# Kernel optimization log

Measured on AMD Instinct MI355X. Metric: run time of the kernel, lower is better.

Reference implementation:

```python
import jax, jax.numpy as jnp
import numpy as np

L, D, H, F = 6, 768, 12, 3072   # layers, d_model, heads, mlp hidden
B, S = 2, 2048                   # batch, seq_len
DH = D // H                      # head dim
EPS = 1e-5


def _layer_norm(x, w, b):
    mu = jnp.mean(x, axis=-1, keepdims=True)
    var = jnp.mean(jnp.square(x - mu), axis=-1, keepdims=True)
    return (x - mu) * jax.lax.rsqrt(var + EPS) * w + b


def setup_inputs() -> dict:
    key = jax.random.key(0)
    ks = jax.random.split(key, 8)
    w = lambda k, shape: jax.random.normal(k, shape, dtype=jnp.float32) * 0.02
    return {
        "x": jax.random.normal(ks[0], (B, S, D), dtype=jnp.float32),
        # attention projections, stacked over layers; weights stored (d_in, d_out)
        "Wq": w(ks[1], (L, D, D)), "bq": jnp.zeros((L, D), jnp.float32),
        "Wk": w(ks[2], (L, D, D)), "bk": jnp.zeros((L, D), jnp.float32),
        "Wv": w(ks[3], (L, D, D)), "bv": jnp.zeros((L, D), jnp.float32),
        "Wo": w(ks[4], (L, D, D)), "bo": jnp.zeros((L, D), jnp.float32),
        "ln1_w": jnp.ones((L, D), jnp.float32), "ln1_b": jnp.zeros((L, D), jnp.float32),
        "W1": w(ks[5], (L, D, F)), "b1": jnp.zeros((L, F), jnp.float32),
        "W2": w(ks[6], (L, F, D)), "b2": jnp.zeros((L, D), jnp.float32),
        "ln2_w": jnp.ones((L, D), jnp.float32), "ln2_b": jnp.zeros((L, D), jnp.float32),
        "lnf_w": jnp.ones((D,), jnp.float32), "lnf_b": jnp.zeros((D,), jnp.float32),
    }


def reference(x, Wq, bq, Wk, bk, Wv, bv, Wo, bo, ln1_w, ln1_b,
              W1, b1, W2, b2, ln2_w, ln2_b, lnf_w, lnf_b):
    scale = DH ** (-0.5)
    for i in range(L):
        # pre-norm MSA block; NB: residual uses the normalized x, as in source
        xn = _layer_norm(x, ln1_w[i], ln1_b[i])
        q = (xn @ Wq[i] + bq[i]).reshape(B, S, H, DH).transpose(0, 2, 1, 3)
        k = (xn @ Wk[i] + bk[i]).reshape(B, S, H, DH).transpose(0, 2, 1, 3)
        v = (xn @ Wv[i] + bv[i]).reshape(B, S, H, DH).transpose(0, 2, 1, 3)
        att = jax.nn.softmax(scale * jnp.einsum('bhqd,bhkd->bhqk', q, k), axis=-1)
        out = jnp.einsum('bhqk,bhkd->bhqd', att, v)
        out = out.transpose(0, 2, 1, 3).reshape(B, S, D)
        x = xn + (out @ Wo[i] + bo[i])
        # pre-norm FFN block; residual uses the normalized x, as in source
        xn2 = _layer_norm(x, ln2_w[i], ln2_b[i])
        h = jax.nn.gelu(xn2 @ W1[i] + b1[i], approximate=False)
        x = xn2 + (h @ W2[i] + b2[i])
    return _layer_norm(x, lnf_w, lnf_b)
```

## Files before the change

### kernel.cpp

```cpp
#include <hip/hip_runtime.h>
#include <stdint.h>

typedef unsigned short u16;
typedef unsigned int   u32;

#define L_N  6
#define D_N  768
#define F_N  3072
#define H_N  12
#define B_N  2
#define S_N  2048
#define BS_N 4096
#define QKV_N 2304
#define CSC  0.18033688011112042f
#define DTHR 11.54f

using bf16x8 = __attribute__((ext_vector_type(8))) short;
using f32x4  = __attribute__((ext_vector_type(4))) float;
using f32x16 = __attribute__((ext_vector_type(16))) float;
using u32x2  = __attribute__((ext_vector_type(2))) unsigned int;

__device__ __forceinline__ u16 f2bf(float f) {
  u32 x = __builtin_bit_cast(u32, f);
  x += 0x7FFFu + ((x >> 16) & 1u);
  return (u16)(x >> 16);
}

__device__ __forceinline__ float bf2f(u16 v) {
  return __builtin_bit_cast(float, (u32)v << 16);
}

__device__ __forceinline__ u32 cvt_pk_bf16(float lo, float hi) {
  u32 r;
  asm("v_cvt_pk_bf16_f32 %0, %1, %2" : "=v"(r) : "v"(lo), "v"(hi));
  return r;
}

#define GLOAD16(g, l)                                                                     \
  __builtin_amdgcn_global_load_lds((const __attribute__((address_space(1))) void*)(g),    \
                                   (__attribute__((address_space(3))) void*)(l), 16, 0, 0)

__global__ __launch_bounds__(256) void transpose_cast_kernel(
    const float* __restrict__ in, u16* __restrict__ out, int K, int N,
    size_t out_lstride, int out_rowoff)
{
  __shared__ float tile[32][33];
  const int l  = blockIdx.z;
  const int n0 = blockIdx.x * 32, k0 = blockIdx.y * 32;
  const int tx = threadIdx.x & 31, ty = threadIdx.x >> 5;
  const float* src = in + (size_t)l * K * N;
  u16* dst = out + (size_t)l * out_lstride + (size_t)out_rowoff * K;
#pragma unroll
  for (int i = 0; i < 4; ++i)
    tile[ty + i * 8][tx] = src[(size_t)(k0 + ty + i * 8) * N + n0 + tx];
  __syncthreads();
#pragma unroll
  for (int i = 0; i < 4; ++i)
    dst[(size_t)(n0 + ty + i * 8) * K + k0 + tx] = f2bf(tile[tx][ty + i * 8]);
}

__global__ __launch_bounds__(256) void concat_bias_kernel(
    const float* __restrict__ bq, const float* __restrict__ bk,
    const float* __restrict__ bv, float* __restrict__ out)
{
  const int i = blockIdx.x * 256 + threadIdx.x;
  const int l = i / QKV_N, c = i - l * QKV_N;
  float v = (c < 768) ? bq[l * 768 + c]
          : (c < 1536) ? bk[l * 768 + c - 768]
                       : bv[l * 768 + c - 1536];
  out[i] = v;
}

template<bool BF16IN>
__global__ __launch_bounds__(256) void ln_kernel(
    const void* __restrict__ xv, const float* __restrict__ w, const float* __restrict__ b,
    float* __restrict__ outF, u16* __restrict__ outB)
{
  const int row = blockIdx.x, tid = threadIdx.x;
  float v[3];
  float s = 0.f;
  if (BF16IN) {
    const u16* xr = (const u16*)xv + (size_t)row * D_N;
#pragma unroll
    for (int i = 0; i < 3; ++i) { v[i] = bf2f(xr[tid + i * 256]); s += v[i]; }
  } else {
    const float* xr = (const float*)xv + (size_t)row * D_N;
#pragma unroll
    for (int i = 0; i < 3; ++i) { v[i] = xr[tid + i * 256]; s += v[i]; }
  }
  __shared__ float red[8];
  const int wave = tid >> 6, lane = tid & 63;
#pragma unroll
  for (int o = 32; o > 0; o >>= 1) s += __shfl_down(s, o, 64);
  if (lane == 0) red[wave] = s;
  __syncthreads();
  const float mu = (red[0] + red[1] + red[2] + red[3]) * (1.f / D_N);
  float d2 = 0.f;
#pragma unroll
  for (int i = 0; i < 3; ++i) { float d = v[i] - mu; d2 += d * d; }
#pragma unroll
  for (int o = 32; o > 0; o >>= 1) d2 += __shfl_down(d2, o, 64);
  if (lane == 0) red[4 + wave] = d2;
  __syncthreads();
  const float var = (red[4] + red[5] + red[6] + red[7]) * (1.f / D_N);
  const float rs = rsqrtf(var + 1e-5f);
#pragma unroll
  for (int i = 0; i < 3; ++i) {
    const int c = tid + i * 256;
    const float o = (v[i] - mu) * rs * w[c] + b[c];
    if (outF) outF[(size_t)row * D_N + c] = o;
    if (outB) outB[(size_t)row * D_N + c] = f2bf(o);
  }
}

template<bool GELU, bool OUTB, bool SCALEQ>
__global__ __launch_bounds__(256) void gemm_kernel(
    const u16* __restrict__ A, const u16* __restrict__ Wt,
    const float* __restrict__ bias,
    u16* __restrict__ outB, int M, int N, int K)
{
  __shared__ __align__(16) u16 As[2][128 * 32];
  __shared__ __align__(16) u16 Bs[2][128 * 32];
  const int tid  = threadIdx.x;
  const int wave = tid >> 6, lane = tid & 63;
  const int lr = lane & 15, lg = lane >> 4;
  const int row0 = blockIdx.x * 128, col0 = blockIdx.y * 128;
  const int wr = (wave >> 1) * 64, wc = (wave & 1) * 64;

  const int cb0 = wave * 64;
  const int cb1 = 256 + wave * 64;
  const int r0s = (cb0 + lane) >> 2, c0s = ((cb0 + lane) & 3) << 3;
  const int r1s = (cb1 + lane) >> 2, c1s = ((cb1 + lane) & 3) << 3;

  f32x4 acc[4][4] = {};

#define STAGE(cbuf, kk)                                                           \
  do {                                                                            \
    GLOAD16(A  + (size_t)(row0 + r0s) * K + (kk) + c0s, &As[cbuf][cb0 * 8]);      \
    GLOAD16(Wt + (size_t)(col0 + r0s) * K + (kk) + c0s, &Bs[cbuf][cb0 * 8]);      \
    GLOAD16(A  + (size_t)(row0 + r1s) * K + (kk) + c1s, &As[cbuf][cb1 * 8]);      \
    GLOAD16(Wt + (size_t)(col0 + r1s) * K + (kk) + c1s, &Bs[cbuf][cb1 * 8]);      \
  } while (0)

  STAGE(0, 0);
  __syncthreads();

  int c = 0;
  for (int k0 = 0; k0 < K; k0 += 32, c ^= 1) {
    if (k0 + 32 < K) STAGE(c ^ 1, k0 + 32);
    bf16x8 af[4], bfr[4];
#pragma unroll
    for (int m = 0; m < 4; ++m)
      af[m] = *(const bf16x8*)&As[c][(wr + m * 16 + lr) * 32 + lg * 8];
#pragma unroll
    for (int n = 0; n < 4; ++n)
      bfr[n] = *(const bf16x8*)&Bs[c][(wc + n * 16 + lr) * 32 + lg * 8];
    __builtin_amdgcn_s_setprio(1);
#pragma unroll
    for (int m = 0; m < 4; ++m)
#pragma unroll
      for (int n = 0; n < 4; ++n)
        acc[m][n] = __builtin_amdgcn_mfma_f32_16x16x32_bf16(af[m], bfr[n], acc[m][n], 0, 0, 0);
    __builtin_amdgcn_s_setprio(0);
    __syncthreads();
  }
#undef STAGE

#pragma unroll
  for (int m = 0; m < 4; ++m)
#pragma unroll
    for (int n = 0; n < 4; ++n) {
      const int col = col0 + wc + n * 16 + lr;
      const float bv = bias[col];
#pragma unroll
      for (int r = 0; r < 4; ++r) {
        const int row = row0 + wr + m * 16 + lg * 4 + r;
        float v = acc[m][n][r] + bv;
        if (GELU) v = 0.5f * v * (1.f + erff(v * 0.70710678118f));
        if (SCALEQ && col < 768) v *= CSC;
        const size_t idx = (size_t)row * N + col;
        if (OUTB) outB[idx] = f2bf(v);
      }
    }
}

__global__ __launch_bounds__(256) void gemm64_kernel(
    const u16* __restrict__ A, const u16* __restrict__ Wt,
    const float* __restrict__ bias, const u16* __restrict__ resid,
    u16* __restrict__ outB, int M, int N, int K)
{
  __shared__ __align__(16) u16 As[2][64 * 32];
  __shared__ __align__(16) u16 Bs[2][64 * 32];
  const int tid  = threadIdx.x;
  const int wave = tid >> 6, lane = tid & 63;
  const int lr = lane & 15, lg = lane >> 4;
  const int row0 = blockIdx.x * 64, col0 = blockIdx.y * 64;
  const int wr = (wave >> 1) * 32, wc = (wave & 1) * 32;

  const int cb = wave * 64;
  const int ch = cb + lane;
  const int rs = ch >> 2, cs = (ch & 3) << 3;

  f32x4 acc[2][2] = {};

#define STAGE64(cbuf, kk)                                                         \
  do {                                                                            \
    GLOAD16(A  + (size_t)(row0 + rs) * K + (kk) + cs, &As[cbuf][cb * 8]);         \
    GLOAD16(Wt + (size_t)(col0 + rs) * K + (kk) + cs, &Bs[cbuf][cb * 8]);         \
  } while (0)

  STAGE64(0, 0);
  __syncthreads();

  int c = 0;
  for (int k0 = 0; k0 < K; k0 += 32, c ^= 1) {
    if (k0 + 32 < K) STAGE64(c ^ 1, k0 + 32);
    bf16x8 af[2], bfr[2];
#pragma unroll
    for (int m = 0; m < 2; ++m)
      af[m] = *(const bf16x8*)&As[c][(wr + m * 16 + lr) * 32 + lg * 8];
#pragma unroll
    for (int n = 0; n < 2; ++n)
      bfr[n] = *(const bf16x8*)&Bs[c][(wc + n * 16 + lr) * 32 + lg * 8];
    __builtin_amdgcn_s_setprio(1);
#pragma unroll
    for (int m = 0; m < 2; ++m)
#pragma unroll
      for (int n = 0; n < 2; ++n)
        acc[m][n] = __builtin_amdgcn_mfma_f32_16x16x32_bf16(af[m], bfr[n], acc[m][n], 0, 0, 0);
    __builtin_amdgcn_s_setprio(0);
    __syncthreads();
  }
#undef STAGE64

#pragma unroll
  for (int m = 0; m < 2; ++m)
#pragma unroll
    for (int n = 0; n < 2; ++n) {
      const int col = col0 + wc + n * 16 + lr;
      const float bv = bias[col];
#pragma unroll
      for (int r = 0; r < 4; ++r) {
        const int row = row0 + wr + m * 16 + lg * 4 + r;
        const size_t idx = (size_t)row * N + col;
        outB[idx] = f2bf(acc[m][n][r] + bv + bf2f(resid[idx]));
      }
    }
}

__global__ __launch_bounds__(256) void attn_kernel(
    const u16* __restrict__ QKV, float* __restrict__ Opart, float* __restrict__ Ml)
{
  constexpr int LDQ = QKV_N;
  constexpr int NT  = S_N / 64;
  __shared__ __align__(16) u16 Ks [64 * 72];
  __shared__ __align__(16) u16 VTs[64 * 72];
  const int tid  = threadIdx.x;
  const int wave = tid >> 6, lane = tid & 63;
  const int l31 = lane & 31, l5 = lane >> 5;
  const int bh = blockIdx.y;
  const int b = bh / H_N, h = bh - b * H_N;
  const int q0 = blockIdx.x * 128;
  const int z  = blockIdx.z;
  const int t0 = z * (NT / 2), t1 = (z + 1) * (NT / 2);
  const size_t rowbase = (size_t)b * S_N * LDQ;
  const u16* Qg = QKV + rowbase + h * 64;
  const u16* Kg = QKV + rowbase + 768 + h * 64;
  const u16* Vg = QKV + rowbase + 1536 + h * 64;

  const int qrow = q0 + wave * 32 + l31;
  bf16x8 qf[4];
#pragma unroll
  for (int ks = 0; ks < 4; ++ks)
    qf[ks] = *(const bf16x8*)(Qg + (size_t)qrow * LDQ + ks * 16 + l5 * 8);

  f32x16 o0 = {}, o1 = {};
  float m = -1e30f, l = 0.f;

  const int kr = tid >> 2, kc = (tid & 3) * 16;
  const int pp = tid >> 3, cg = tid & 7;

  const u16* gk0 = Kg + (size_t)(t0 * 64 + kr) * LDQ + kc;
  const u16* gv0 = Vg + (size_t)(t0 * 64 + 2 * pp) * LDQ + cg * 8;
  uint4 nk0 = *(const uint4*)gk0, nk1 = *(const uint4*)(gk0 + 8);
  uint4 nv0 = *(const uint4*)gv0, nv1 = *(const uint4*)(gv0 + LDQ);

  for (int t = t0; t < t1; ++t) {
    __syncthreads();
    {
      *(uint4*)&Ks[kr * 72 + kc]     = nk0;
      *(uint4*)&Ks[kr * 72 + kc + 8] = nk1;
      const u16* a0 = (const u16*)&nv0;
      const u16* a1 = (const u16*)&nv1;
#pragma unroll
      for (int j = 0; j < 8; ++j) {
        const int jj = (j + cg) & 7;
        *(u32*)&VTs[(cg * 8 + jj) * 72 + 2 * pp] = (u32)a0[jj] | ((u32)a1[jj] << 16);
      }
    }
    __syncthreads();

    if (t + 1 < t1) {
      const u16* gk1 = Kg + (size_t)((t + 1) * 64 + kr) * LDQ + kc;
      const u16* gv1 = Vg + (size_t)((t + 1) * 64 + 2 * pp) * LDQ + cg * 8;
      nk0 = *(const uint4*)gk1; nk1 = *(const uint4*)(gk1 + 8);
      nv0 = *(const uint4*)gv1; nv1 = *(const uint4*)(gv1 + LDQ);
    }

    f32x16 sv0 = {}, sv1 = {};
    __builtin_amdgcn_s_setprio(1);
#pragma unroll
    for (int ks = 0; ks < 4; ++ks) {
      const bf16x8 kf0 = *(const bf16x8*)&Ks[(l31)      * 72 + ks * 16 + l5 * 8];
      const bf16x8 kf1 = *(const bf16x8*)&Ks[(32 + l31) * 72 + ks * 16 + l5 * 8];
      sv0 = __builtin_amdgcn_mfma_f32_32x32x16_bf16(kf0, qf[ks], sv0, 0, 0, 0);
      sv1 = __builtin_amdgcn_mfma_f32_32x32x16_bf16(kf1, qf[ks], sv1, 0, 0, 0);
    }
    __builtin_amdgcn_s_setprio(0);

    float mx = sv0[0];
#pragma unroll
    for (int i = 0; i < 16; ++i) mx = fmaxf(mx, sv0[i]);
#pragma unroll
    for (int i = 0; i < 16; ++i) mx = fmaxf(mx, sv1[i]);
    {
      const u32 mb = __builtin_bit_cast(u32, mx);
      const u32x2 rr = __builtin_amdgcn_permlane32_swap(mb, mb, false, false);
      mx = fmaxf(__builtin_bit_cast(float, rr[0]), __builtin_bit_cast(float, rr[1]));
    }
    if (!__all(mx - m <= DTHR)) {
      const float mn = fmaxf(m, mx);
      const float al = __builtin_amdgcn_exp2f(m - mn);
      m = mn;
      l *= al;
#pragma unroll
      for (int i = 0; i < 16; ++i) { o0[i] *= al; o1[i] *= al; }
    }
    float rs = 0.f;
#pragma unroll
    for (int i = 0; i < 16; ++i) {
      const float e = __builtin_amdgcn_exp2f(sv0[i] - m);
      sv0[i] = e; rs += e;
    }
#pragma unroll
    for (int i = 0; i < 16; ++i) {
      const float e = __builtin_amdgcn_exp2f(sv1[i] - m);
      sv1[i] = e; rs += e;
    }
    {
      const u32 sb = __builtin_bit_cast(u32, rs);
      const u32x2 rr = __builtin_amdgcn_permlane32_swap(sb, sb, false, false);
      rs = __builtin_bit_cast(float, rr[0]) + __builtin_bit_cast(float, rr[1]);
    }
    l += rs;

    bf16x8 pb[4];
#pragma unroll
    for (int kb = 0; kb < 2; ++kb) {
      const f32x16& p = kb ? sv1 : sv0;
#pragma unroll
      for (int half = 0; half < 2; ++half) {
        const int o8 = half * 8;
        const u32 a0 = cvt_pk_bf16(p[o8 + 0], p[o8 + 1]);
        const u32 b0 = cvt_pk_bf16(p[o8 + 4], p[o8 + 5]);
        const u32 a1 = cvt_pk_bf16(p[o8 + 2], p[o8 + 3]);
        const u32 b1 = cvt_pk_bf16(p[o8 + 6], p[o8 + 7]);
        const u32x2 r0 = __builtin_amdgcn_permlane32_swap(a0, b0, false, false);
        const u32x2 r1 = __builtin_amdgcn_permlane32_swap(a1, b1, false, false);
        u32 w[4] = { r0[0], r1[0], r0[1], r1[1] };
        pb[kb * 2 + half] = __builtin_bit_cast(bf16x8, *(const uint4*)w);
      }
    }

    __builtin_amdgcn_s_setprio(1);
#pragma unroll
    for (int ks2 = 0; ks2 < 4; ++ks2) {
      const bf16x8 vf0 = *(const bf16x8*)&VTs[(l31)      * 72 + ks2 * 16 + l5 * 8];
      const bf16x8 vf1 = *(const bf16x8*)&VTs[(32 + l31) * 72 + ks2 * 16 + l5 * 8];
      o0 = __builtin_amdgcn_mfma_f32_32x32x16_bf16(vf0, pb[ks2], o0, 0, 0, 0);
      o1 = __builtin_amdgcn_mfma_f32_32x32x16_bf16(vf1, pb[ks2], o1, 0, 0, 0);
    }
    __builtin_amdgcn_s_setprio(0);
  }

  float* op = Opart + (((size_t)z * B_N * H_N + bh) * S_N + qrow) * 64;
#pragma unroll
  for (int r = 0; r < 16; r += 2) {
    const int dh = (r & 3) + 8 * (r >> 2) + 4 * l5;
    *(float2*)(op + dh)      = float2{o0[r], o0[r + 1]};
    *(float2*)(op + dh + 32) = float2{o1[r], o1[r + 1]};
  }
  if (l5 == 0) {
    float* mlp = Ml + (((size_t)z * B_N * H_N + bh) * S_N + qrow) * 2;
    mlp[0] = m; mlp[1] = l;
  }
}

__global__ __launch_bounds__(256) void attn_combine_kernel(
    const float* __restrict__ Opart, const float* __restrict__ Ml, u16* __restrict__ O)
{
  constexpr size_t HALF = (size_t)B_N * H_N * S_N;
  const int tid = threadIdx.x;
  const int lane = tid & 63, grp = tid >> 6;
  const size_t row = (size_t)blockIdx.x * 4 + grp;
  const float* p0 = Opart + row * 64;
  const float* p1 = p0 + HALF * 64;
  const float m0 = Ml[row * 2], l0 = Ml[row * 2 + 1];
  const float m1 = Ml[(row + HALF) * 2], l1 = Ml[(row + HALF) * 2 + 1];
  const float mm = fmaxf(m0, m1);
  const float a0 = __builtin_amdgcn_exp2f(m0 - mm);
  const float a1 = __builtin_amdgcn_exp2f(m1 - mm);
  const float inv = 1.f / (a0 * l0 + a1 * l1);
  const float o = (a0 * p0[lane] + a1 * p1[lane]) * inv;
  const int bh = (int)(row / S_N), s = (int)(row % S_N);
  const int b = bh / H_N, h = bh - b * H_N;
  O[((size_t)b * S_N + s) * D_N + h * 64 + lane] = f2bf(o);
}

extern "C" void kernel_launch(void* const* d_in, const int* in_sizes, int n_in,
                              void* d_out, int out_size, void* d_ws, size_t ws_size,
                              hipStream_t stream)
{
  (void)in_sizes; (void)n_in; (void)out_size; (void)ws_size;
  const float* x0   = (const float*)d_in[0];
  const float* Wq   = (const float*)d_in[1];
  const float* bq   = (const float*)d_in[2];
  const float* Wk   = (const float*)d_in[3];
  const float* bk   = (const float*)d_in[4];
  const float* Wv   = (const float*)d_in[5];
  const float* bv   = (const float*)d_in[6];
  const float* Wo   = (const float*)d_in[7];
  const float* bo   = (const float*)d_in[8];
  const float* ln1w = (const float*)d_in[9];
  const float* ln1b = (const float*)d_in[10];
  const float* W1   = (const float*)d_in[11];
  const float* b1   = (const float*)d_in[12];
  const float* W2   = (const float*)d_in[13];
  const float* b2   = (const float*)d_in[14];
  const float* ln2w = (const float*)d_in[15];
  const float* ln2b = (const float*)d_in[16];
  const float* lnfw = (const float*)d_in[17];
  const float* lnfb = (const float*)d_in[18];

  char* ws = (char*)d_ws;
  size_t off = 0;
  auto alloc = [&](size_t bytes) {
    char* p = ws + off; off += (bytes + 255) & ~(size_t)255; return p;
  };
  u16*   wqkv_t = (u16*)alloc((size_t)L_N * QKV_N * D_N * 2);
  u16*   wo_t   = (u16*)alloc((size_t)L_N * D_N * D_N * 2);
  u16*   w1_t   = (u16*)alloc((size_t)L_N * D_N * F_N * 2);
  u16*   w2_t   = (u16*)alloc((size_t)L_N * D_N * F_N * 2);
  float* bqkv   = (float*)alloc((size_t)L_N * QKV_N * 4);
  u16*   x_b    = (u16*)alloc((size_t)BS_N * D_N * 2);
  u16*   xn_b   = (u16*)alloc((size_t)BS_N * D_N * 2);
  u16*   qkvb   = (u16*)alloc((size_t)BS_N * QKV_N * 2);
  u16*   ab     = (u16*)alloc((size_t)BS_N * D_N * 2);
  u16*   hb     = (u16*)alloc((size_t)BS_N * F_N * 2);
  float* ml     = (float*)alloc((size_t)2 * B_N * H_N * S_N * 2 * 4);
  float* opart  = (float*)hb;

  const size_t dd = (size_t)D_N * D_N, qs = (size_t)QKV_N * D_N, df = (size_t)D_N * F_N;
  transpose_cast_kernel<<<dim3(D_N/32, D_N/32, L_N), 256, 0, stream>>>(Wq, wqkv_t, D_N, D_N, qs, 0);
  transpose_cast_kernel<<<dim3(D_N/32, D_N/32, L_N), 256, 0, stream>>>(Wk, wqkv_t, D_N, D_N, qs, 768);
  transpose_cast_kernel<<<dim3(D_N/32, D_N/32, L_N), 256, 0, stream>>>(Wv, wqkv_t, D_N, D_N, qs, 1536);
  transpose_cast_kernel<<<dim3(D_N/32, D_N/32, L_N), 256, 0, stream>>>(Wo, wo_t, D_N, D_N, dd, 0);
  transpose_cast_kernel<<<dim3(F_N/32, D_N/32, L_N), 256, 0, stream>>>(W1, w1_t, D_N, F_N, df, 0);
  transpose_cast_kernel<<<dim3(D_N/32, F_N/32, L_N), 256, 0, stream>>>(W2, w2_t, F_N, D_N, df, 0);
  concat_bias_kernel<<<(L_N * QKV_N) / 256, 256, 0, stream>>>(bq, bk, bv, bqkv);

  const dim3 gQKV(BS_N / 128, QKV_N / 128);
  const dim3 gF  (BS_N / 128, F_N / 128);
  const dim3 g64 (BS_N / 64,  D_N / 64);
  const dim3 gA  (S_N / 128, B_N * H_N, 2);

  for (int i = 0; i < L_N; ++i) {
    if (i == 0)
      ln_kernel<false><<<BS_N, 256, 0, stream>>>(x0, ln1w, ln1b, nullptr, xn_b);
    else
      ln_kernel<true><<<BS_N, 256, 0, stream>>>(x_b, ln1w + i * D_N, ln1b + i * D_N, nullptr, xn_b);
    gemm_kernel<false,true,true><<<gQKV, 256, 0, stream>>>(
        xn_b, wqkv_t + (size_t)i * qs, bqkv + (size_t)i * QKV_N, qkvb, BS_N, QKV_N, D_N);
    attn_kernel<<<gA, 256, 0, stream>>>(qkvb, opart, ml);
    attn_combine_kernel<<<(B_N * H_N * S_N) / 4, 256, 0, stream>>>(opart, ml, ab);
    gemm64_kernel<<<g64, 256, 0, stream>>>(
        ab, wo_t + (size_t)i * dd, bo + i * D_N, xn_b, x_b, BS_N, D_N, D_N);
    ln_kernel<true><<<BS_N, 256, 0, stream>>>(x_b, ln2w + i * D_N, ln2b + i * D_N, nullptr, xn_b);
    gemm_kernel<true,true,false><<<gF, 256, 0, stream>>>(
        xn_b, w1_t + (size_t)i * df, b1 + i * F_N, hb, BS_N, F_N, D_N);
    gemm64_kernel<<<g64, 256, 0, stream>>>(
        hb, w2_t + (size_t)i * df, b2 + i * D_N, xn_b, x_b, BS_N, D_N, F_N);
  }
  ln_kernel<true><<<BS_N, 256, 0, stream>>>(x_b, lnfw, lnfb, (float*)d_out, nullptr);
}
```

Before: 1.334 ms.

## Fuse split-K attention combine into attention kernel via last-block atomic flag

Removes the separate attn_combine kernel. Each attention block bumps an atomic counter for its (bh, q-tile), and the second block to finish merges the two partial outputs and writes the bf16 result. It also turns the row max and sum reductions into trees to shorten dependency chains. This saves one launch per layer and a pass over the partials, at the cost of threadfences, an atomic, and a per-call kernel that zeroes the flags.

```diff
diff --git a/kernel.cpp b/kernel.cpp
--- a/kernel.cpp
+++ b/kernel.cpp
@@ -14,6 +14,8 @@
 #define QKV_N 2304
 #define CSC  0.18033688011112042f
 #define DTHR 11.54f
+#define NQT  (S_N / 128)
+#define NFLG (B_N * H_N * NQT)
 
 using bf16x8 = __attribute__((ext_vector_type(8))) short;
 using f32x4  = __attribute__((ext_vector_type(4))) float;
@@ -39,6 +41,12 @@
 #define GLOAD16(g, l)                                                                     \
   __builtin_amdgcn_global_load_lds((const __attribute__((address_space(1))) void*)(g),    \
                                    (__attribute__((address_space(3))) void*)(l), 16, 0, 0)
+
+__global__ __launch_bounds__(256) void zero_flags_kernel(u32* __restrict__ f, int n)
+{
+  const int i = blockIdx.x * 256 + threadIdx.x;
+  if (i < n) f[i] = 0;
+}
 
 __global__ __launch_bounds__(256) void transpose_cast_kernel(
     const float* __restrict__ in, u16* __restrict__ out, int K, int N,
@@ -249,10 +257,12 @@
 }
 
 __global__ __launch_bounds__(256) void attn_kernel(
-    const u16* __restrict__ QKV, float* __restrict__ Opart, float* __restrict__ Ml)
+    const u16* __restrict__ QKV, float* __restrict__ Opart, float* __restrict__ Ml,
+    u16* __restrict__ O, u32* __restrict__ flags)
 {
   constexpr int LDQ = QKV_N;
   constexpr int NT  = S_N / 64;
+  constexpr int BH  = B_N * H_N;
   __shared__ __align__(16) u16 Ks [64 * 72];
   __shared__ __align__(16) u16 VTs[64 * 72];
   const int tid  = threadIdx.x;
@@ -318,11 +328,13 @@
     }
     __builtin_amdgcn_s_setprio(0);
 
-    float mx = sv0[0];
-#pragma unroll
-    for (int i = 0; i < 16; ++i) mx = fmaxf(mx, sv0[i]);
-#pragma unroll
-    for (int i = 0; i < 16; ++i) mx = fmaxf(mx, sv1[i]);
+    float t8[8];
+#pragma unroll
+    for (int i = 0; i < 8; ++i)
+      t8[i] = fmaxf(fmaxf(sv0[i], sv0[i + 8]), fmaxf(sv1[i], sv1[i + 8]));
+#pragma unroll
+    for (int i = 0; i < 4; ++i) t8[i] = fmaxf(t8[i], t8[i + 4]);
+    float mx = fmaxf(fmaxf(t8[0], t8[2]), fmaxf(t8[1], t8[3]));
     {
       const u32 mb = __builtin_bit_cast(u32, mx);
       const u32x2 rr = __builtin_amdgcn_permlane32_swap(mb, mb, false, false);
@@ -336,17 +348,17 @@
 #pragma unroll
       for (int i = 0; i < 16; ++i) { o0[i] *= al; o1[i] *= al; }
     }
-    float rs = 0.f;
-#pragma unroll
-    for (int i = 0; i < 16; ++i) {
-      const float e = __builtin_amdgcn_exp2f(sv0[i] - m);
-      sv0[i] = e; rs += e;
-    }
-#pragma unroll
-    for (int i = 0; i < 16; ++i) {
-      const float e = __builtin_amdgcn_exp2f(sv1[i] - m);
-      sv1[i] = e; rs += e;
-    }
+#pragma unroll
+    for (int i = 0; i < 16; ++i) sv0[i] = __builtin_amdgcn_exp2f(sv0[i] - m);
+#pragma unroll
+    for (int i = 0; i < 16; ++i) sv1[i] = __builtin_amdgcn_exp2f(sv1[i] - m);
+    float s8[8];
+#pragma unroll
+    for (int i = 0; i < 8; ++i)
+      s8[i] = (sv0[i] + sv0[i + 8]) + (sv1[i] + sv1[i + 8]);
+#pragma unroll
+    for (int i = 0; i < 4; ++i) s8[i] += s8[i + 4];
+    float rs = (s8[0] + s8[2]) + (s8[1] + s8[3]);
     {
       const u32 sb = __builtin_bit_cast(u32, rs);
       const u32x2 rr = __builtin_amdgcn_permlane32_swap(sb, sb, false, false);
@@ -383,7 +395,7 @@
     __builtin_amdgcn_s_setprio(0);
   }
 
-  float* op = Opart + (((size_t)z * B_N * H_N + bh) * S_N + qrow) * 64;
+  float* op = Opart + (((size_t)z * BH + bh) * S_N + qrow) * 64;
 #pragma unroll
   for (int r = 0; r < 16; r += 2) {
     const int dh = (r & 3) + 8 * (r >> 2) + 4 * l5;
@@ -391,30 +403,41 @@
     *(float2*)(op + dh + 32) = float2{o1[r], o1[r + 1]};
   }
   if (l5 == 0) {
-    float* mlp = Ml + (((size_t)z * B_N * H_N + bh) * S_N + qrow) * 2;
+    float* mlp = Ml + (((size_t)z * BH + bh) * S_N + qrow) * 2;
     mlp[0] = m; mlp[1] = l;
   }
-}
-
-__global__ __launch_bounds__(256) void attn_combine_kernel(
-    const float* __restrict__ Opart, const float* __restrict__ Ml, u16* __restrict__ O)
-{
-  constexpr size_t HALF = (size_t)B_N * H_N * S_N;
-  const int tid = threadIdx.x;
-  const int lane = tid & 63, grp = tid >> 6;
-  const size_t row = (size_t)blockIdx.x * 4 + grp;
-  const float* p0 = Opart + row * 64;
-  const float* p1 = p0 + HALF * 64;
-  const float m0 = Ml[row * 2], l0 = Ml[row * 2 + 1];
-  const float m1 = Ml[(row + HALF) * 2], l1 = Ml[(row + HALF) * 2 + 1];
+
+  __shared__ int s_last;
+  __syncthreads();
+  if (tid == 0) {
+    __threadfence();
+    const u32 old = atomicAdd(&flags[bh * NQT + blockIdx.x], 1u);
+    __threadfence();
+    s_last = (old == 1u);
+  }
+  __syncthreads();
+  if (!s_last) return;
+
+  const float* P0 = Opart + (((size_t)0 * BH + bh) * S_N + q0) * 64;
+  const float* P1 = Opart + (((size_t)1 * BH + bh) * S_N + q0) * 64;
+  const float* M0 = Ml + (((size_t)0 * BH + bh) * S_N + q0) * 2;
+  const float* M1 = Ml + (((size_t)1 * BH + bh) * S_N + q0) * 2;
+  const int rr = tid >> 1, cc = (tid & 1) * 32;
+  const float m0 = M0[rr * 2], l0 = M0[rr * 2 + 1];
+  const float m1 = M1[rr * 2], l1 = M1[rr * 2 + 1];
   const float mm = fmaxf(m0, m1);
   const float a0 = __builtin_amdgcn_exp2f(m0 - mm);
   const float a1 = __builtin_amdgcn_exp2f(m1 - mm);
   const float inv = 1.f / (a0 * l0 + a1 * l1);
-  const float o = (a0 * p0[lane] + a1 * p1[lane]) * inv;
-  const int bh = (int)(row / S_N), s = (int)(row % S_N);
-  const int b = bh / H_N, h = bh - b * H_N;
-  O[((size_t)b * S_N + s) * D_N + h * 64 + lane] = f2bf(o);
+  const float* r0p = P0 + rr * 64 + cc;
+  const float* r1p = P1 + rr * 64 + cc;
+  u16* orow = O + (size_t)(b * S_N + q0 + rr) * D_N + h * 64 + cc;
+#pragma unroll
+  for (int j = 0; j < 32; j += 2) {
+    const float x0 = (a0 * r0p[j]     + a1 * r1p[j])     * inv;
+    const float x1 = (a0 * r0p[j + 1] + a1 * r1p[j + 1]) * inv;
+    *(u32*)(orow + j) = cvt_pk_bf16(x0, x1);
+  }
 }
 
 extern "C" void kernel_launch(void* const* d_in, const int* in_sizes, int n_in,
@@ -458,7 +481,10 @@
   u16*   ab     = (u16*)alloc((size_t)BS_N * D_N * 2);
   u16*   hb     = (u16*)alloc((size_t)BS_N * F_N * 2);
   float* ml     = (float*)alloc((size_t)2 * B_N * H_N * S_N * 2 * 4);
+  u32*   flags  = (u32*)alloc((size_t)L_N * NFLG * 4);
   float* opart  = (float*)hb;
+
+  zero_flags_kernel<<<(L_N * NFLG + 255) / 256, 256, 0, stream>>>(flags, L_N * NFLG);
 
   const size_t dd = (size_t)D_N * D_N, qs = (size_t)QKV_N * D_N, df = (size_t)D_N * F_N;
   transpose_cast_kernel<<<dim3(D_N/32, D_N/32, L_N), 256, 0, stream>>>(Wq, wqkv_t, D_N, D_N, qs, 0);
@@ -472,7 +498,7 @@
   const dim3 gQKV(BS_N / 128, QKV_N / 128);
   const dim3 gF  (BS_N / 128, F_N / 128);
   const dim3 g64 (BS_N / 64,  D_N / 64);
-  const dim3 gA  (S_N / 128, B_N * H_N, 2);
+  const dim3 gA  (NQT, B_N * H_N, 2);
 
   for (int i = 0; i < L_N; ++i) {
     if (i == 0)
@@ -481,8 +507,7 @@
       ln_kernel<true><<<BS_N, 256, 0, stream>>>(x_b, ln1w + i * D_N, ln1b + i * D_N, nullptr, xn_b);
     gemm_kernel<false,true,true><<<gQKV, 256, 0, stream>>>(
         xn_b, wqkv_t + (size_t)i * qs, bqkv + (size_t)i * QKV_N, qkvb, BS_N, QKV_N, D_N);
-    attn_kernel<<<gA, 256, 0, stream>>>(qkvb, opart, ml);
-    attn_combine_kernel<<<(B_N * H_N * S_N) / 4, 256, 0, stream>>>(opart, ml, ab);
+    attn_kernel<<<gA, 256, 0, stream>>>(qkvb, opart, ml, ab, flags + (size_t)i * NFLG);
     gemm64_kernel<<<g64, 256, 0, stream>>>(
         ab, wo_t + (size_t)i * dd, bo + i * D_N, xn_b, x_b, BS_N, D_N, D_N);
     ln_kernel<true><<<BS_N, 256, 0, stream>>>(x_b, ln2w + i * D_N, ln2b + i * D_N, nullptr, xn_b);
```

New measurement: 1.667 ms. 1.25x slower.
